# Optimization experiments

Measured on AMD Instinct MI355X. Metric: run time of the kernel, lower is better.

Reference implementation:

```python
import jax, jax.numpy as jnp
import numpy as np

DIM = 2048
RANK = 128


def _xavier_uniform(key, shape, gain=0.5):
    fan_out, fan_in = shape
    limit = gain * np.sqrt(6.0 / (fan_in + fan_out))
    return jax.random.uniform(key, shape, jnp.float32, -limit, limit)


def setup_inputs() -> dict:
    key = jax.random.key(0)
    ks = jax.random.split(key, 6)
    T, B = 1024, 16
    x = jax.random.normal(ks[0], (T, B, DIM), jnp.float32)
    h0 = jax.random.normal(ks[1], (B, DIM), jnp.float32)
    U_x = _xavier_uniform(ks[2], (DIM, RANK))
    V_x = _xavier_uniform(ks[3], (RANK, DIM))
    U_d = _xavier_uniform(ks[4], (DIM, RANK))
    V_d = _xavier_uniform(ks[5], (RANK, DIM))
    r_h = jnp.full((DIM,), 0.9, jnp.float32)
    r_delta = jnp.full((DIM,), 0.1, jnp.float32)
    b = jnp.zeros((DIM,), jnp.float32)
    b_delta = jnp.full((DIM,), -2.0, jnp.float32)
    b_gate = jnp.zeros((DIM,), jnp.float32)
    return {"x": x, "h0": h0, "U_x": U_x, "V_x": V_x, "U_d": U_d, "V_d": V_d,
            "r_h": r_h, "r_delta": r_delta, "b": b, "b_delta": b_delta, "b_gate": b_gate}


def reference(x, h0, U_x, V_x, U_d, V_d, r_h, r_delta, b, b_delta, b_gate):
    # Precompute input projections for all timesteps (batched low-rank GEMMs):
    # W(x) = U @ (V @ x)  ->  [T,B,D]
    wx = jnp.einsum('tbd,rd,or->tbo', x, V_x, U_x)
    wd = jnp.einsum('tbd,rd,or->tbo', x, V_d, U_d)

    def step(h_prev, inp):
        x_t, wx_t, wd_t = inp
        cand = jnp.tanh(r_h * h_prev + wx_t + b)
        delta = jax.nn.sigmoid(wd_t + r_delta * h_prev + b_delta)
        h_new = (1.0 - delta) * h_prev + delta * cand
        g = h_new + x_t + b_gate
        out = h_new * (g * jax.nn.sigmoid(g))  # silu gate
        return h_new, (out, h_new)

    _, (output, hs) = jax.lax.scan(step, h0, (x, wx, wd))
    h = jnp.concatenate([h0[None], hs], axis=0)  # [T+1,B,D]
    return output, h
```

## Files before the change

### kernel.cpp

```cpp
#include <hip/hip_runtime.h>

#define DIMN 2048
#define RANKN 128
#define TT 1024
#define BBATCH 16
#define BD (BBATCH * DIMN)
#define CH 16
#define PADW 132

typedef __attribute__((ext_vector_type(4))) float floatx4;
typedef __attribute__((ext_vector_type(8))) short short8;

__device__ __forceinline__ short f2bf(float f) {
    unsigned u = __float_as_uint(f);
    unsigned r = (u + 0x7FFFu + ((u >> 16) & 1u)) >> 16;
    return (short)r;
}
__device__ __forceinline__ float fast_sigmoid(float z) {
    return 1.0f / (1.0f + __expf(-z));
}
__device__ __forceinline__ float fast_tanh(float z) {
    return 1.0f - 2.0f / (__expf(2.0f * z) + 1.0f);
}

__global__ __launch_bounds__(256)
void prep_vb(const float* __restrict__ Vx, const float* __restrict__ Vd,
             short* __restrict__ Vb) {
    const int gid = blockIdx.x * 256 + threadIdx.x;
    const size_t base = (size_t)gid * 8;
    const size_t half = (size_t)RANKN * DIMN;
    const float* src = (base < half) ? Vx : Vd;
    const size_t off = (base < half) ? base : (base - half);
    float4 a = *(const float4*)(src + off);
    float4 c = *(const float4*)(src + off + 4);
    short8 v;
    v[0] = f2bf(a.x); v[1] = f2bf(a.y); v[2] = f2bf(a.z); v[3] = f2bf(a.w);
    v[4] = f2bf(c.x); v[5] = f2bf(c.y); v[6] = f2bf(c.z); v[7] = f2bf(c.w);
    *(short8*)(Vb + base) = v;
}

__global__ __launch_bounds__(256, 2)
void gemm_xv(const float* __restrict__ X, const short* __restrict__ Vb,
             short* __restrict__ xvb) {
    constexpr int PADK = 40;
    __shared__ short As[32 * PADK];
    __shared__ short Bs[2][128 * PADK];

    const int m0 = blockIdx.x * 32;
    const int tid = threadIdx.x;
    const int wave = tid >> 6;
    const int lane = tid & 63;
    const int lr = lane & 15;
    const int q  = lane >> 4;
    const int mat = wave >> 1;
    const int wn  = (wave & 1) * 64;

    floatx4 acc[2][4] = {};

    for (int k0 = 0; k0 < DIMN; k0 += 32) {
        {
            int r = tid >> 3, c = (tid & 7) * 4;
            float4 v = *(const float4*)(X + (size_t)(m0 + r) * DIMN + k0 + c);
            *(short4*)&As[r * PADK + c] =
                make_short4(f2bf(v.x), f2bf(v.y), f2bf(v.z), f2bf(v.w));
        }
        #pragma unroll
        for (int i = 0; i < 4; ++i) {
            int u = tid + i * 256;
            int bm = u >> 9;
            int rem = u & 511;
            int r = rem >> 2, c8 = (rem & 3) * 8;
            short8 v = *(const short8*)(Vb + ((size_t)bm * RANKN + r) * DIMN + k0 + c8);
            *(short8*)&Bs[bm][r * PADK + c8] = v;
        }
        __syncthreads();

        short8 af[2], bfr[4];
        #pragma unroll
        for (int mi = 0; mi < 2; ++mi)
            af[mi] = *(const short8*)&As[(mi * 16 + lr) * PADK + q * 8];
        #pragma unroll
        for (int nj = 0; nj < 4; ++nj)
            bfr[nj] = *(const short8*)&Bs[mat][(wn + nj * 16 + lr) * PADK + q * 8];

        #pragma unroll
        for (int mi = 0; mi < 2; ++mi)
            #pragma unroll
            for (int nj = 0; nj < 4; ++nj)
                acc[mi][nj] = __builtin_amdgcn_mfma_f32_16x16x32_bf16(
                    af[mi], bfr[nj], acc[mi][nj], 0, 0, 0);
        __syncthreads();
    }

    #pragma unroll
    for (int mi = 0; mi < 2; ++mi)
        #pragma unroll
        for (int nj = 0; nj < 4; ++nj)
            #pragma unroll
            for (int r = 0; r < 4; ++r) {
                int row = m0 + mi * 16 + q * 4 + r;
                int col = mat * RANKN + wn + nj * 16 + lr;
                xvb[(size_t)row * 256 + col] = f2bf(acc[mi][nj][r]);
            }
}

__global__ __launch_bounds__(256, 1)
void fused_scan(const short* __restrict__ xvb, const float* __restrict__ x,
                const float* __restrict__ h0,
                const float* __restrict__ Ux, const float* __restrict__ Ud,
                const float* __restrict__ r_h, const float* __restrict__ r_delta,
                const float* __restrict__ bvec, const float* __restrict__ b_delta,
                const float* __restrict__ b_gate,
                float* __restrict__ obuf, float* __restrict__ hbuf) {
    __shared__ float wxs[2][CH * PADW];
    __shared__ float wds[2][CH * PADW];
    __shared__ float hs [2][CH * PADW];

    const int id   = blockIdx.x;
    const int xcd  = id & 7;
    const int slot = id >> 3;
    const int b  = xcd + 8 * (slot & 1);
    const int d0 = (slot >> 1) * 128;

    const int tid = threadIdx.x;
    const int wave = tid >> 6;
    const int lane = tid & 63;
    const int lr = lane & 15;
    const int q  = lane >> 4;
    const int wn = (wave & 1) * 64;

    const int cix = tid & 127;
    const int d   = d0 + cix;
    const size_t xoff = (size_t)b * DIMN + d;

    const int dq  = tid & 31;
    const int tof = (tid >> 5) & 3;
    const size_t xoffF = (size_t)b * DIMN + d0 + dq * 4;

    short8 uf[2][4][4];
    short8 afp[2][4], afn[2][4];
    float4 xpre[4], xnew[4];
    float4 bg4 = {};
    float h = 0.f, rh = 0.f, rd = 0.f, bb = 0.f, bdl = 0.f;

    if (wave < 2) {
        #pragma unroll
        for (int mat = 0; mat < 2; ++mat) {
            const float* Up = mat ? Ud : Ux;
            #pragma unroll
            for (int nj = 0; nj < 4; ++nj) {
                const size_t dd = (size_t)(d0 + wn + nj * 16 + lr);
                #pragma unroll
                for (int ks = 0; ks < 4; ++ks) {
                    const int k = ks * 32 + q * 8;
                    float4 u0 = *(const float4*)&Up[dd * RANKN + k];
                    float4 u1 = *(const float4*)&Up[dd * RANKN + k + 4];
                    short8 v;
                    v[0] = f2bf(u0.x); v[1] = f2bf(u0.y);
                    v[2] = f2bf(u0.z); v[3] = f2bf(u0.w);
                    v[4] = f2bf(u1.x); v[5] = f2bf(u1.y);
                    v[6] = f2bf(u1.z); v[7] = f2bf(u1.w);
                    uf[mat][nj][ks] = v;
                }
            }
        }
        {
            const size_t row = (size_t)lr * BBATCH + b;
            #pragma unroll
            for (int mat = 0; mat < 2; ++mat)
                #pragma unroll
                for (int ks = 0; ks < 4; ++ks)
                    afp[mat][ks] = *(const short8*)
                        &xvb[row * 256 + mat * RANKN + ks * 32 + q * 8];
        }
        bg4 = *(const float4*)&b_gate[d0 + dq * 4];
    } else {
        rh  = r_h[d];  rd  = r_delta[d];
        bb  = bvec[d]; bdl = b_delta[d];
        h = h0[xoff];
        hbuf[xoff] = h;
    }

    for (int i = 0; i < 66; ++i) {
        if (wave < 2) {
            if (i < 64) {
                const int pb = i & 1;
                #pragma unroll
                for (int mat = 0; mat < 2; ++mat) {
                    float* outp = mat ? wds[pb] : wxs[pb];
                    #pragma unroll
                    for (int nj = 0; nj < 4; ++nj) {
                        floatx4 acc = {};
                        #pragma unroll
                        for (int ks = 0; ks < 4; ++ks)
                            acc = __builtin_amdgcn_mfma_f32_16x16x32_bf16(
                                afp[mat][ks], uf[mat][nj][ks], acc, 0, 0, 0);
                        #pragma unroll
                        for (int r = 0; r < 4; ++r)
                            outp[(q * 4 + r) * PADW + wn + nj * 16 + lr] = acc[r];
                    }
                }
            }
            if (i < 63) {
                const size_t row = (size_t)((i + 1) * CH + lr) * BBATCH + b;
                #pragma unroll
                for (int mat = 0; mat < 2; ++mat)
                    #pragma unroll
                    for (int ks = 0; ks < 4; ++ks)
                        afn[mat][ks] = *(const short8*)
                            &xvb[row * 256 + mat * RANKN + ks * 32 + q * 8];
            }
            if (i >= 1 && i < 65) {
                const int tb = (i - 1) * CH;
                #pragma unroll
                for (int jj = 0; jj < 4; ++jj)
                    xnew[jj] = *(const float4*)
                        &x[(size_t)(tb + jj * 4 + tof) * BD + xoffF];
            }
            if (i >= 2) {
                const int j = i - 2;
                const int fb = j & 1;
                const int tb = j * CH;
                #pragma unroll
                for (int jj = 0; jj < 4; ++jj) {
                    const int t = jj * 4 + tof;
                    const float4 hv = *(const float4*)&hs[fb][t * PADW + dq * 4];
                    const float4 xv = xpre[jj];
                    float4 ov;
                    {
                        float g0 = hv.x + xv.x + bg4.x;
                        ov.x = hv.x * (g0 * fast_sigmoid(g0));
                        float g1 = hv.y + xv.y + bg4.y;
                        ov.y = hv.y * (g1 * fast_sigmoid(g1));
                        float g2 = hv.z + xv.z + bg4.z;
                        ov.z = hv.z * (g2 * fast_sigmoid(g2));
                        float g3 = hv.w + xv.w + bg4.w;
                        ov.w = hv.w * (g3 * fast_sigmoid(g3));
                    }
                    *(float4*)&obuf[(size_t)(tb + t) * BD + xoffF] = ov;
                    *(float4*)&hbuf[(size_t)(tb + t + 1) * BD + xoffF] = hv;
                }
            }
            if (i < 63) {
                #pragma unroll
                for (int mat = 0; mat < 2; ++mat)
                    #pragma unroll
                    for (int ks = 0; ks < 4; ++ks)
                        afp[mat][ks] = afn[mat][ks];
            }
            if (i >= 1 && i < 65) {
                #pragma unroll
                for (int jj = 0; jj < 4; ++jj)
                    xpre[jj] = xnew[jj];
            }
        } else if (i >= 1 && i < 65) {
            const int pb = (i - 1) & 1;
            float wxr[CH], wdr[CH];
            #pragma unroll
            for (int s = 0; s < CH; ++s) {
                wxr[s] = wxs[pb][s * PADW + cix];
                wdr[s] = wds[pb][s * PADW + cix];
            }
            #pragma unroll
            for (int s = 0; s < CH; ++s) {
                const float cand  = fast_tanh(rh * h + wxr[s] + bb);
                const float delta = fast_sigmoid(wdr[s] + rd * h + bdl);
                h = (1.0f - delta) * h + delta * cand;
                hs[pb][s * PADW + cix] = h;
            }
        }
        __syncthreads();
    }
}

extern "C" void kernel_launch(void* const* d_in, const int* in_sizes, int n_in,
                              void* d_out, int out_size, void* d_ws, size_t ws_size,
                              hipStream_t stream) {
    const float* x       = (const float*)d_in[0];
    const float* h0      = (const float*)d_in[1];
    const float* U_x     = (const float*)d_in[2];
    const float* V_x     = (const float*)d_in[3];
    const float* U_d     = (const float*)d_in[4];
    const float* V_d     = (const float*)d_in[5];
    const float* r_h     = (const float*)d_in[6];
    const float* r_delta = (const float*)d_in[7];
    const float* bvec    = (const float*)d_in[8];
    const float* b_delta = (const float*)d_in[9];
    const float* b_gate  = (const float*)d_in[10];

    float* obuf = (float*)d_out;
    float* hbuf = obuf + (size_t)TT * BD;
    short* xvb  = (short*)d_ws;
    short* Vb   = xvb + (size_t)TT * BBATCH * 256;

    prep_vb<<<256, 256, 0, stream>>>(V_x, V_d, Vb);

    gemm_xv<<<TT * BBATCH / 32, 256, 0, stream>>>(x, Vb, xvb);

    fused_scan<<<256, 256, 0, stream>>>(xvb, x, h0, U_x, U_d,
                                        r_h, r_delta, bvec, b_delta, b_gate,
                                        obuf, hbuf);
}
```

Measured before the change: 550.1 us.

## Rewrite xV GEMM as register-only single-wave kernel and halve scan block width

The x·V projection GEMM drops shared-memory staging and barriers. Each single-wave block now loads A and B fragments straight from global memory into registers, double-buffered across two K-halves, and computes all 256 output columns. The fused scan kernel is split into 512 blocks of 128 threads, each covering 64 channels with one MFMA wave and one recurrence wave, to spread the serial scan over more CUs. The cost is heavy register use in the GEMM (32 accumulators plus prefetch buffers), and the GEMM no longer shares B fragments across waves through LDS.

Result: slower. 579.6 us (+5.4%).

```diff
diff --git a/kernel.cpp b/kernel.cpp
--- a/kernel.cpp
+++ b/kernel.cpp
@@ -6,7 +6,7 @@
 #define BBATCH 16
 #define BD (BBATCH * DIMN)
 #define CH 16
-#define PADW 132
+#define PADW 68
 
 typedef __attribute__((ext_vector_type(4))) float floatx4;
 typedef __attribute__((ext_vector_type(8))) short short8;
@@ -39,72 +39,78 @@
     *(short8*)(Vb + base) = v;
 }
 
-__global__ __launch_bounds__(256, 2)
+__global__ __launch_bounds__(64, 1)
 void gemm_xv(const float* __restrict__ X, const short* __restrict__ Vb,
              short* __restrict__ xvb) {
-    constexpr int PADK = 40;
-    __shared__ short As[32 * PADK];
-    __shared__ short Bs[2][128 * PADK];
-
-    const int m0 = blockIdx.x * 32;
-    const int tid = threadIdx.x;
-    const int wave = tid >> 6;
-    const int lane = tid & 63;
+    const int lane = threadIdx.x;
     const int lr = lane & 15;
     const int q  = lane >> 4;
-    const int mat = wave >> 1;
-    const int wn  = (wave & 1) * 64;
-
-    floatx4 acc[2][4] = {};
-
-    for (int k0 = 0; k0 < DIMN; k0 += 32) {
-        {
-            int r = tid >> 3, c = (tid & 7) * 4;
-            float4 v = *(const float4*)(X + (size_t)(m0 + r) * DIMN + k0 + c);
-            *(short4*)&As[r * PADK + c] =
-                make_short4(f2bf(v.x), f2bf(v.y), f2bf(v.z), f2bf(v.w));
-        }
+    const int m0 = blockIdx.x * 32;
+
+    const float* ap = X  + (size_t)(m0 + lr) * DIMN + q * 8;
+    const short* bp = Vb + (size_t)lr * DIMN + q * 8;
+
+    floatx4 acc[2][16] = {};
+    float4 aA[2][2], aB[2][2];
+    short8 bA[16], bB[16];
+
+    #pragma unroll
+    for (int mi = 0; mi < 2; ++mi) {
+        const float* am = ap + (size_t)mi * 16 * DIMN;
+        aA[mi][0] = *(const float4*)(am);
+        aA[mi][1] = *(const float4*)(am + 4);
+        aB[mi][0] = *(const float4*)(am + 32);
+        aB[mi][1] = *(const float4*)(am + 36);
+    }
+    #pragma unroll
+    for (int nj = 0; nj < 16; ++nj) {
+        const short* bn = bp + (size_t)nj * 16 * DIMN;
+        bA[nj] = *(const short8*)(bn);
+        bB[nj] = *(const short8*)(bn + 32);
+    }
+
+    auto step = [&](float4 (&xa)[2][2], short8 (&bset)[16], int knext, bool pf) {
+        short8 af[2];
         #pragma unroll
-        for (int i = 0; i < 4; ++i) {
-            int u = tid + i * 256;
-            int bm = u >> 9;
-            int rem = u & 511;
-            int r = rem >> 2, c8 = (rem & 3) * 8;
-            short8 v = *(const short8*)(Vb + ((size_t)bm * RANKN + r) * DIMN + k0 + c8);
-            *(short8*)&Bs[bm][r * PADK + c8] = v;
-        }
-        __syncthreads();
-
-        short8 af[2], bfr[4];
+        for (int mi = 0; mi < 2; ++mi) {
+            af[mi][0] = f2bf(xa[mi][0].x); af[mi][1] = f2bf(xa[mi][0].y);
+            af[mi][2] = f2bf(xa[mi][0].z); af[mi][3] = f2bf(xa[mi][0].w);
+            af[mi][4] = f2bf(xa[mi][1].x); af[mi][5] = f2bf(xa[mi][1].y);
+            af[mi][6] = f2bf(xa[mi][1].z); af[mi][7] = f2bf(xa[mi][1].w);
+            if (pf) {
+                const float* am = ap + (size_t)mi * 16 * DIMN + knext;
+                xa[mi][0] = *(const float4*)(am);
+                xa[mi][1] = *(const float4*)(am + 4);
+            }
+        }
         #pragma unroll
-        for (int mi = 0; mi < 2; ++mi)
-            af[mi] = *(const short8*)&As[(mi * 16 + lr) * PADK + q * 8];
+        for (int nj = 0; nj < 16; ++nj) {
+            short8 bv = bset[nj];
+            if (pf) bset[nj] = *(const short8*)(bp + (size_t)nj * 16 * DIMN + knext);
+            #pragma unroll
+            for (int mi = 0; mi < 2; ++mi)
+                acc[mi][nj] = __builtin_amdgcn_mfma_f32_16x16x32_bf16(
+                    af[mi], bv, acc[mi][nj], 0, 0, 0);
+        }
+    };
+
+    for (int k0 = 0; k0 < DIMN; k0 += 64) {
+        step(aA, bA, k0 + 64, k0 + 64 < DIMN);
+        step(aB, bB, k0 + 96, k0 + 96 < DIMN);
+    }
+
+    #pragma unroll
+    for (int mi = 0; mi < 2; ++mi) {
+        short* cp = xvb + (size_t)(m0 + mi * 16 + q * 4) * 256 + lr;
         #pragma unroll
-        for (int nj = 0; nj < 4; ++nj)
-            bfr[nj] = *(const short8*)&Bs[mat][(wn + nj * 16 + lr) * PADK + q * 8];
-
-        #pragma unroll
-        for (int mi = 0; mi < 2; ++mi)
-            #pragma unroll
-            for (int nj = 0; nj < 4; ++nj)
-                acc[mi][nj] = __builtin_amdgcn_mfma_f32_16x16x32_bf16(
-                    af[mi], bfr[nj], acc[mi][nj], 0, 0, 0);
-        __syncthreads();
-    }
-
-    #pragma unroll
-    for (int mi = 0; mi < 2; ++mi)
-        #pragma unroll
-        for (int nj = 0; nj < 4; ++nj)
-            #pragma unroll
-            for (int r = 0; r < 4; ++r) {
-                int row = m0 + mi * 16 + q * 4 + r;
-                int col = mat * RANKN + wn + nj * 16 + lr;
-                xvb[(size_t)row * 256 + col] = f2bf(acc[mi][nj][r]);
-            }
-}
-
-__global__ __launch_bounds__(256, 1)
+        for (int nj = 0; nj < 16; ++nj)
+            #pragma unroll
+            for (int r = 0; r < 4; ++r)
+                cp[(size_t)r * 256 + nj * 16] = f2bf(acc[mi][nj][r]);
+    }
+}
+
+__global__ __launch_bounds__(128, 1)
 void fused_scan(const short* __restrict__ xvb, const float* __restrict__ x,
                 const float* __restrict__ h0,
                 const float* __restrict__ Ux, const float* __restrict__ Ud,
@@ -119,22 +125,19 @@
     const int id   = blockIdx.x;
     const int xcd  = id & 7;
     const int slot = id >> 3;
-    const int b  = xcd + 8 * (slot & 1);
-    const int d0 = (slot >> 1) * 128;
-
-    const int tid = threadIdx.x;
+    const int b  = xcd * 2 + (slot & 1);
+    const int d0 = (slot >> 1) * 64;
+
+    const int tid  = threadIdx.x;
     const int wave = tid >> 6;
     const int lane = tid & 63;
     const int lr = lane & 15;
     const int q  = lane >> 4;
-    const int wn = (wave & 1) * 64;
-
-    const int cix = tid & 127;
-    const int d   = d0 + cix;
+
+    const int d = d0 + lane;
     const size_t xoff = (size_t)b * DIMN + d;
-
-    const int dq  = tid & 31;
-    const int tof = (tid >> 5) & 3;
+    const int dq  = lane & 15;
+    const int tof = lane >> 4;
     const size_t xoffF = (size_t)b * DIMN + d0 + dq * 4;
 
     short8 uf[2][4][4];
@@ -143,13 +146,13 @@
     float4 bg4 = {};
     float h = 0.f, rh = 0.f, rd = 0.f, bb = 0.f, bdl = 0.f;
 
-    if (wave < 2) {
+    if (wave == 0) {
         #pragma unroll
         for (int mat = 0; mat < 2; ++mat) {
             const float* Up = mat ? Ud : Ux;
             #pragma unroll
             for (int nj = 0; nj < 4; ++nj) {
-                const size_t dd = (size_t)(d0 + wn + nj * 16 + lr);
+                const size_t dd = (size_t)(d0 + nj * 16 + lr);
                 #pragma unroll
                 for (int ks = 0; ks < 4; ++ks) {
                     const int k = ks * 32 + q * 8;
@@ -182,7 +185,7 @@
     }
 
     for (int i = 0; i < 66; ++i) {
-        if (wave < 2) {
+        if (wave == 0) {
             if (i < 64) {
                 const int pb = i & 1;
                 #pragma unroll
@@ -197,7 +200,7 @@
                                 afp[mat][ks], uf[mat][nj][ks], acc, 0, 0, 0);
                         #pragma unroll
                         for (int r = 0; r < 4; ++r)
-                            outp[(q * 4 + r) * PADW + wn + nj * 16 + lr] = acc[r];
+                            outp[(q * 4 + r) * PADW + nj * 16 + lr] = acc[r];
                     }
                 }
             }
@@ -258,15 +261,15 @@
             float wxr[CH], wdr[CH];
             #pragma unroll
             for (int s = 0; s < CH; ++s) {
-                wxr[s] = wxs[pb][s * PADW + cix];
-                wdr[s] = wds[pb][s * PADW + cix];
+                wxr[s] = wxs[pb][s * PADW + lane];
+                wdr[s] = wds[pb][s * PADW + lane];
             }
             #pragma unroll
             for (int s = 0; s < CH; ++s) {
                 const float cand  = fast_tanh(rh * h + wxr[s] + bb);
                 const float delta = fast_sigmoid(wdr[s] + rd * h + bdl);
                 h = (1.0f - delta) * h + delta * cand;
-                hs[pb][s * PADW + cix] = h;
+                hs[pb][s * PADW + lane] = h;
             }
         }
         __syncthreads();
@@ -295,9 +298,9 @@
 
     prep_vb<<<256, 256, 0, stream>>>(V_x, V_d, Vb);
 
-    gemm_xv<<<TT * BBATCH / 32, 256, 0, stream>>>(x, Vb, xvb);
-
-    fused_scan<<<256, 256, 0, stream>>>(xvb, x, h0, U_x, U_d,
+    gemm_xv<<<TT * BBATCH / 32, 64, 0, stream>>>(x, Vb, xvb);
+
+    fused_scan<<<512, 128, 0, stream>>>(xvb, x, h0, U_x, U_d,
                                         r_h, r_delta, bvec, b_delta, b_gate,
                                         obuf, hbuf);
 }
```

## Restructure fused scan into single-wave blocks with no block barriers

Applied to the files above, without the earlier changes.

The fused scan kernel moves from 256 blocks of four specialised waves (two MFMA producer waves, two recurrence waves, with ping-pong LDS buffers and __syncthreads) to 512 single-wave blocks, each covering 64 channels of one batch row. Each wave computes its own U-projection with MFMA, writes it to LDS, waits with an explicit lgkmcnt, then runs the recurrence and the silu output directly, double-buffering the next chunk's xvb fragments and x values in registers. This removes block-level barriers and the producer/consumer handoff, and spreads the work over twice as many blocks. In exchange the per-chunk MFMA work now sits serially before the recurrence instead of overlapping with it, output stores become scalar instead of float4, and uf fragments take more registers per wave.

After: 576.5 us. 1.05x slower.

```diff
diff --git a/kernel.cpp b/kernel.cpp
--- a/kernel.cpp
+++ b/kernel.cpp
@@ -6,7 +6,7 @@
 #define BBATCH 16
 #define BD (BBATCH * DIMN)
 #define CH 16
-#define PADW 132
+#define PADW 68
 
 typedef __attribute__((ext_vector_type(4))) float floatx4;
 typedef __attribute__((ext_vector_type(8))) short short8;
@@ -104,7 +104,7 @@
             }
 }
 
-__global__ __launch_bounds__(256, 1)
+__global__ __launch_bounds__(64, 1)
 void fused_scan(const short* __restrict__ xvb, const float* __restrict__ x,
                 const float* __restrict__ h0,
                 const float* __restrict__ Ux, const float* __restrict__ Ud,
@@ -112,164 +112,123 @@
                 const float* __restrict__ bvec, const float* __restrict__ b_delta,
                 const float* __restrict__ b_gate,
                 float* __restrict__ obuf, float* __restrict__ hbuf) {
-    __shared__ float wxs[2][CH * PADW];
-    __shared__ float wds[2][CH * PADW];
-    __shared__ float hs [2][CH * PADW];
+    __shared__ float wxs[CH * PADW];
+    __shared__ float wds[CH * PADW];
 
     const int id   = blockIdx.x;
     const int xcd  = id & 7;
     const int slot = id >> 3;
-    const int b  = xcd + 8 * (slot & 1);
-    const int d0 = (slot >> 1) * 128;
-
-    const int tid = threadIdx.x;
-    const int wave = tid >> 6;
-    const int lane = tid & 63;
+    const int b  = xcd * 2 + (slot & 1);
+    const int d0 = (slot >> 1) * 64;
+
+    const int lane = threadIdx.x;
     const int lr = lane & 15;
     const int q  = lane >> 4;
-    const int wn = (wave & 1) * 64;
-
-    const int cix = tid & 127;
-    const int d   = d0 + cix;
-    const size_t xoff = (size_t)b * DIMN + d;
-
-    const int dq  = tid & 31;
-    const int tof = (tid >> 5) & 3;
-    const size_t xoffF = (size_t)b * DIMN + d0 + dq * 4;
+
+    const int d = d0 + lane;
+    const size_t xo = (size_t)b * DIMN + d;
 
     short8 uf[2][4][4];
-    short8 afp[2][4], afn[2][4];
-    float4 xpre[4], xnew[4];
-    float4 bg4 = {};
-    float h = 0.f, rh = 0.f, rd = 0.f, bb = 0.f, bdl = 0.f;
-
-    if (wave < 2) {
-        #pragma unroll
-        for (int mat = 0; mat < 2; ++mat) {
-            const float* Up = mat ? Ud : Ux;
-            #pragma unroll
-            for (int nj = 0; nj < 4; ++nj) {
-                const size_t dd = (size_t)(d0 + wn + nj * 16 + lr);
-                #pragma unroll
-                for (int ks = 0; ks < 4; ++ks) {
-                    const int k = ks * 32 + q * 8;
-                    float4 u0 = *(const float4*)&Up[dd * RANKN + k];
-                    float4 u1 = *(const float4*)&Up[dd * RANKN + k + 4];
-                    short8 v;
-                    v[0] = f2bf(u0.x); v[1] = f2bf(u0.y);
-                    v[2] = f2bf(u0.z); v[3] = f2bf(u0.w);
-                    v[4] = f2bf(u1.x); v[5] = f2bf(u1.y);
-                    v[6] = f2bf(u1.z); v[7] = f2bf(u1.w);
-                    uf[mat][nj][ks] = v;
-                }
+    #pragma unroll
+    for (int mat = 0; mat < 2; ++mat) {
+        const float* Up = mat ? Ud : Ux;
+        #pragma unroll
+        for (int nj = 0; nj < 4; ++nj) {
+            const size_t dd = (size_t)(d0 + nj * 16 + lr);
+            #pragma unroll
+            for (int ks = 0; ks < 4; ++ks) {
+                const int k = ks * 32 + q * 8;
+                float4 u0 = *(const float4*)&Up[dd * RANKN + k];
+                float4 u1 = *(const float4*)&Up[dd * RANKN + k + 4];
+                short8 v;
+                v[0] = f2bf(u0.x); v[1] = f2bf(u0.y);
+                v[2] = f2bf(u0.z); v[3] = f2bf(u0.w);
+                v[4] = f2bf(u1.x); v[5] = f2bf(u1.y);
+                v[6] = f2bf(u1.z); v[7] = f2bf(u1.w);
+                uf[mat][nj][ks] = v;
             }
         }
-        {
-            const size_t row = (size_t)lr * BBATCH + b;
+    }
+
+    const float rh  = r_h[d];
+    const float rd  = r_delta[d];
+    const float bb  = bvec[d];
+    const float bdl = b_delta[d];
+    const float bg  = b_gate[d];
+    float h = h0[xo];
+    hbuf[xo] = h;
+
+    short8 afA[2][4], afB[2][4];
+    float  xqA[CH],  xqB[CH];
+    {
+        const size_t row = (size_t)lr * BBATCH + b;
+        #pragma unroll
+        for (int mat = 0; mat < 2; ++mat)
+            #pragma unroll
+            for (int ks = 0; ks < 4; ++ks)
+                afA[mat][ks] = *(const short8*)
+                    &xvb[row * 256 + mat * RANKN + ks * 32 + q * 8];
+        #pragma unroll
+        for (int s = 0; s < CH; ++s)
+            xqA[s] = x[(size_t)s * BD + xo];
+    }
+
+    auto body = [&](int ch, short8 (&afU)[2][4], short8 (&afP)[2][4],
+                    float (&xU)[CH], float (&xP)[CH]) {
+        if (ch < 63) {
+            const size_t row = (size_t)((ch + 1) * CH + lr) * BBATCH + b;
             #pragma unroll
             for (int mat = 0; mat < 2; ++mat)
                 #pragma unroll
                 for (int ks = 0; ks < 4; ++ks)
-                    afp[mat][ks] = *(const short8*)
+                    afP[mat][ks] = *(const short8*)
                         &xvb[row * 256 + mat * RANKN + ks * 32 + q * 8];
-        }
-        bg4 = *(const float4*)&b_gate[d0 + dq * 4];
-    } else {
-        rh  = r_h[d];  rd  = r_delta[d];
-        bb  = bvec[d]; bdl = b_delta[d];
-        h = h0[xoff];
-        hbuf[xoff] = h;
-    }
-
-    for (int i = 0; i < 66; ++i) {
-        if (wave < 2) {
-            if (i < 64) {
-                const int pb = i & 1;
+            const size_t xb0 = (size_t)(ch + 1) * CH * BD + xo;
+            #pragma unroll
+            for (int s = 0; s < CH; ++s)
+                xP[s] = x[xb0 + (size_t)s * BD];
+        }
+
+        #pragma unroll
+        for (int mat = 0; mat < 2; ++mat) {
+            float* outp = mat ? wds : wxs;
+            #pragma unroll
+            for (int nj = 0; nj < 4; ++nj) {
+                floatx4 acc = {};
                 #pragma unroll
-                for (int mat = 0; mat < 2; ++mat) {
-                    float* outp = mat ? wds[pb] : wxs[pb];
-                    #pragma unroll
-                    for (int nj = 0; nj < 4; ++nj) {
-                        floatx4 acc = {};
-                        #pragma unroll
-                        for (int ks = 0; ks < 4; ++ks)
-                            acc = __builtin_amdgcn_mfma_f32_16x16x32_bf16(
-                                afp[mat][ks], uf[mat][nj][ks], acc, 0, 0, 0);
-                        #pragma unroll
-                        for (int r = 0; r < 4; ++r)
-                            outp[(q * 4 + r) * PADW + wn + nj * 16 + lr] = acc[r];
-                    }
-                }
+                for (int ks = 0; ks < 4; ++ks)
+                    acc = __builtin_amdgcn_mfma_f32_16x16x32_bf16(
+                        afU[mat][ks], uf[mat][nj][ks], acc, 0, 0, 0);
+                #pragma unroll
+                for (int r = 0; r < 4; ++r)
+                    outp[(q * 4 + r) * PADW + nj * 16 + lr] = acc[r];
             }
-            if (i < 63) {
-                const size_t row = (size_t)((i + 1) * CH + lr) * BBATCH + b;
-                #pragma unroll
-                for (int mat = 0; mat < 2; ++mat)
-                    #pragma unroll
-                    for (int ks = 0; ks < 4; ++ks)
-                        afn[mat][ks] = *(const short8*)
-                            &xvb[row * 256 + mat * RANKN + ks * 32 + q * 8];
-            }
-            if (i >= 1 && i < 65) {
-                const int tb = (i - 1) * CH;
-                #pragma unroll
-                for (int jj = 0; jj < 4; ++jj)
-                    xnew[jj] = *(const float4*)
-                        &x[(size_t)(tb + jj * 4 + tof) * BD + xoffF];
-            }
-            if (i >= 2) {
-                const int j = i - 2;
-                const int fb = j & 1;
-                const int tb = j * CH;
-                #pragma unroll
-                for (int jj = 0; jj < 4; ++jj) {
-                    const int t = jj * 4 + tof;
-                    const float4 hv = *(const float4*)&hs[fb][t * PADW + dq * 4];
-                    const float4 xv = xpre[jj];
-                    float4 ov;
-                    {
-                        float g0 = hv.x + xv.x + bg4.x;
-                        ov.x = hv.x * (g0 * fast_sigmoid(g0));
-                        float g1 = hv.y + xv.y + bg4.y;
-                        ov.y = hv.y * (g1 * fast_sigmoid(g1));
-                        float g2 = hv.z + xv.z + bg4.z;
-                        ov.z = hv.z * (g2 * fast_sigmoid(g2));
-                        float g3 = hv.w + xv.w + bg4.w;
-                        ov.w = hv.w * (g3 * fast_sigmoid(g3));
-                    }
-                    *(float4*)&obuf[(size_t)(tb + t) * BD + xoffF] = ov;
-                    *(float4*)&hbuf[(size_t)(tb + t + 1) * BD + xoffF] = hv;
-                }
-            }
-            if (i < 63) {
-                #pragma unroll
-                for (int mat = 0; mat < 2; ++mat)
-                    #pragma unroll
-                    for (int ks = 0; ks < 4; ++ks)
-                        afp[mat][ks] = afn[mat][ks];
-            }
-            if (i >= 1 && i < 65) {
-                #pragma unroll
-                for (int jj = 0; jj < 4; ++jj)
-                    xpre[jj] = xnew[jj];
-            }
-        } else if (i >= 1 && i < 65) {
-            const int pb = (i - 1) & 1;
-            float wxr[CH], wdr[CH];
-            #pragma unroll
-            for (int s = 0; s < CH; ++s) {
-                wxr[s] = wxs[pb][s * PADW + cix];
-                wdr[s] = wds[pb][s * PADW + cix];
-            }
-            #pragma unroll
-            for (int s = 0; s < CH; ++s) {
-                const float cand  = fast_tanh(rh * h + wxr[s] + bb);
-                const float delta = fast_sigmoid(wdr[s] + rd * h + bdl);
-                h = (1.0f - delta) * h + delta * cand;
-                hs[pb][s * PADW + cix] = h;
-            }
-        }
-        __syncthreads();
+        }
+        asm volatile("s_waitcnt lgkmcnt(0)" ::: "memory");
+
+        float wxr[CH], wdr[CH];
+        #pragma unroll
+        for (int s = 0; s < CH; ++s) {
+            wxr[s] = wxs[s * PADW + lane];
+            wdr[s] = wds[s * PADW + lane];
+        }
+
+        const size_t tb = (size_t)ch * CH * BD + xo;
+        #pragma unroll
+        for (int s = 0; s < CH; ++s) {
+            const float cand  = fast_tanh(rh * h + wxr[s] + bb);
+            const float delta = fast_sigmoid(wdr[s] + rd * h + bdl);
+            h = (1.0f - delta) * h + delta * cand;
+            const float gg = h + xU[s] + bg;
+            obuf[tb + (size_t)s * BD] = h * (gg * fast_sigmoid(gg));
+            hbuf[tb + (size_t)(s + 1) * BD] = h;
+        }
+    };
+
+    #pragma unroll 1
+    for (int ii = 0; ii < 32; ++ii) {
+        body(2 * ii,     afA, afB, xqA, xqB);
+        body(2 * ii + 1, afB, afA, xqB, xqA);
     }
 }
 
@@ -297,7 +256,7 @@
 
     gemm_xv<<<TT * BBATCH / 32, 256, 0, stream>>>(x, Vb, xvb);
 
-    fused_scan<<<256, 256, 0, stream>>>(xvb, x, h0, U_x, U_d,
-                                        r_h, r_delta, bvec, b_delta, b_gate,
-                                        obuf, hbuf);
-}
+    fused_scan<<<512, 64, 0, stream>>>(xvb, x, h0, U_x, U_d,
+                                       r_h, r_delta, bvec, b_delta, b_gate,
+                                       obuf, hbuf);
+}
```
